# Kernel tuning notes

Measured on AMD Instinct MI355X. Metric: run time of the kernel, lower is better.

## Reference

```python
import jax, jax.numpy as jnp
import numpy as np

B = 32        # num graphs
N = 512       # nodes per graph (equal-sized blocks)
HID = 512     # hidden_dim
H = 8         # num_heads
E = 262144    # num edges
ED = 16       # edge feature dim


def setup_inputs() -> dict:
    key = jax.random.key(0)
    ks = jax.random.split(key, 12)
    x = jax.random.normal(ks[0], (B * N, HID), jnp.float32)
    # contiguous, sorted graph assignment (equal-sized graphs)
    batch = jnp.repeat(jnp.arange(B, dtype=jnp.int64), N)
    # within-graph random edges
    g = jax.random.randint(ks[1], (E,), 0, B)
    src = g * N + jax.random.randint(ks[2], (E,), 0, N)
    dst = g * N + jax.random.randint(ks[3], (E,), 0, N)
    edge_index = jnp.stack([src, dst]).astype(jnp.int64)
    edge_attr = jax.random.normal(ks[4], (E, ED), jnp.float32)
    s = 1.0 / np.sqrt(HID).astype(np.float32)
    Wq = jax.random.normal(ks[5], (HID, HID), jnp.float32) * s
    Wk = jax.random.normal(ks[6], (HID, HID), jnp.float32) * s
    Wv = jax.random.normal(ks[7], (HID, HID), jnp.float32) * s
    Wo = jax.random.normal(ks[8], (HID, HID), jnp.float32) * s
    We = jax.random.normal(ks[9], (ED, H), jnp.float32) * (1.0 / np.sqrt(ED).astype(np.float32))
    bq = jnp.zeros((HID,), jnp.float32)
    bk = jnp.zeros((HID,), jnp.float32)
    bv = jnp.zeros((HID,), jnp.float32)
    bo = jnp.zeros((HID,), jnp.float32)
    be = jnp.zeros((H,), jnp.float32)
    return dict(x=x, batch=batch, edge_index=edge_index, edge_attr=edge_attr,
                Wq=Wq, bq=bq, Wk=Wk, bk=bk, Wv=Wv, bv=bv, Wo=Wo, bo=bo,
                We=We, be=be, num_graphs=B)


def reference(x, batch, edge_index, edge_attr, Wq, bq, Wk, bk, Wv, bv, Wo, bo, We, be, num_graphs):
    n_total, hid = x.shape
    n = n_total // num_graphs           # nodes per graph (equal blocks)
    hd = hid // H                       # head_dim
    scale = 1.0 / jnp.sqrt(jnp.asarray(hd, x.dtype))
    q = (x @ Wq + bq).reshape(num_graphs, n, H, hd)
    k = (x @ Wk + bk).reshape(num_graphs, n, H, hd)
    v = (x @ Wv + bv).reshape(num_graphs, n, H, hd)
    # per-graph dense scores: [B, n(query), m(key), H]
    attn = jnp.einsum('bnhd,bmhd->bnmh', q, k) * scale
    # edge-bias scatter-add (edges are intra-graph; local coords via div/mod)
    eb = edge_attr @ We + be                      # [E, H]
    b_idx = edge_index[0] // n
    loc_src = edge_index[0] % n
    loc_dst = edge_index[1] % n
    attn = attn.at[b_idx, loc_src, loc_dst].add(eb)
    # softmax over key axis (torch dim=1 of 'nmh' == axis 2 here)
    attn = jax.nn.softmax(attn, axis=2)
    out = jnp.einsum('bnmh,bmhd->bnhd', attn, v).reshape(n_total, hid)
    return out @ Wo + bo
```

## Files before the change

### kernel.cpp

```cpp
#include <hip/hip_runtime.h>
#include <stdint.h>

typedef unsigned short u16;
typedef __bf16 bf16x8 __attribute__((ext_vector_type(8)));
typedef short  short8 __attribute__((ext_vector_type(8)));
typedef float  f32x4  __attribute__((ext_vector_type(4)));
typedef float  float4v __attribute__((ext_vector_type(4)));
typedef uint32_t u32x2 __attribute__((ext_vector_type(2)));

#define NG    32
#define NPG   512
#define HIDD  512
#define NH    8
#define HD    64
#define NE    262144
#define NNODE (NG*NPG)

__device__ __forceinline__ float fexp2(float x) { return __builtin_amdgcn_exp2f(x); }

__device__ __forceinline__ u16 f2bf(float f) {
  union { float f; uint32_t u; } x; x.f = f;
  uint32_t r = x.u + 0x7FFFu + ((x.u >> 16) & 1u);
  return (u16)(r >> 16);
}
__device__ __forceinline__ float bf2f(u16 b) {
  union { uint32_t u; float f; } x; x.u = ((uint32_t)b) << 16;
  return x.f;
}
__device__ __forceinline__ uint32_t pkbf(float a, float b) {
  __bf16 x = (__bf16)a, y = (__bf16)b;
  return (uint32_t)__builtin_bit_cast(u16, x) | ((uint32_t)__builtin_bit_cast(u16, y) << 16);
}
__device__ __forceinline__ bf16x8 ldfrag(const u16* p) {
  short8 t = *(const short8*)p;
  return __builtin_bit_cast(bf16x8, t);
}
__device__ __forceinline__ f32x4 mfma16(bf16x8 a, bf16x8 b, f32x4 c) {
  return __builtin_amdgcn_mfma_f32_16x16x32_bf16(a, b, c, 0, 0, 0);
}
__device__ __forceinline__ void gl2lds16(const void* g, void* l) {
  __builtin_amdgcn_global_load_lds((const __attribute__((address_space(1))) void*)g,
                                   (__attribute__((address_space(3))) void*)l, 16, 0, 0);
}
__device__ __forceinline__ void st(u16* p, float v)   { *p = f2bf(v); }
__device__ __forceinline__ void st(float* p, float v) { *p = v; }


__global__ void k_cast_x(const float* __restrict__ x, u16* __restrict__ xb) {
  size_t i = ((size_t)blockIdx.x * 256 + threadIdx.x) * 8;
  float4v v0 = *(const float4v*)(x + i);
  float4v v1 = *(const float4v*)(x + i + 4);
  short8 r;
  r[0]=(short)f2bf(v0[0]); r[1]=(short)f2bf(v0[1]); r[2]=(short)f2bf(v0[2]); r[3]=(short)f2bf(v0[3]);
  r[4]=(short)f2bf(v1[0]); r[5]=(short)f2bf(v1[1]); r[6]=(short)f2bf(v1[2]); r[7]=(short)f2bf(v1[3]);
  *(short8*)(xb + i) = r;
}

__global__ void k_transw(const float* __restrict__ W0, const float* __restrict__ W1,
                         const float* __restrict__ W2, const float* __restrict__ W3,
                         u16* __restrict__ wt) {
  const float* W = blockIdx.z==0 ? W0 : blockIdx.z==1 ? W1 : blockIdx.z==2 ? W2 : W3;
  u16* out = wt + (size_t)blockIdx.z * HIDD * HIDD;
  __shared__ float tl[32][33];
  int tx = threadIdx.x, ty = threadIdx.y;
  int x0 = blockIdx.x * 32, y0 = blockIdx.y * 32;
  #pragma unroll
  for (int i = 0; i < 4; ++i) tl[ty + i*8][tx] = W[(size_t)(y0 + ty + i*8) * HIDD + x0 + tx];
  __syncthreads();
  #pragma unroll
  for (int i = 0; i < 4; ++i) out[(size_t)(x0 + ty + i*8) * HIDD + (y0 + tx)] = f2bf(tl[tx][ty + i*8]);
}

__global__ void k_count2(const int* __restrict__ ei, int* __restrict__ counts) {
  int e = blockIdx.x * 256 + threadIdx.x;
  int src = ei[e];
  int dl  = ei[NE + e] & (NPG - 1);
  atomicAdd(&counts[src * 8 + (dl >> 6)], 1);
}

__global__ void k_scan_a(const int* __restrict__ counts, int* __restrict__ rowstart,
                         int* __restrict__ bsum) {
  __shared__ int arr[256];
  int t = threadIdx.x;
  int i = blockIdx.x * 256 + t;
  int c = counts[i];
  arr[t] = c;
  __syncthreads();
  for (int off = 1; off < 256; off <<= 1) {
    int v = (t >= off) ? arr[t - off] : 0;
    __syncthreads();
    arr[t] += v;
    __syncthreads();
  }
  rowstart[i] = arr[t] - c;
  if (t == 255) bsum[blockIdx.x] = arr[255];
}
__global__ void k_scan_b(int* __restrict__ bsum) {
  __shared__ int arr[512];
  int t = threadIdx.x;
  int c = bsum[t];
  arr[t] = c;
  __syncthreads();
  for (int off = 1; off < 512; off <<= 1) {
    int v = (t >= off) ? arr[t - off] : 0;
    __syncthreads();
    arr[t] += v;
    __syncthreads();
  }
  bsum[t] = arr[t] - c;
}
__global__ void k_scan_c(const int* __restrict__ bsum, int* __restrict__ rowstart) {
  int i = blockIdx.x * 256 + threadIdx.x;
  rowstart[i] += bsum[blockIdx.x];
  if (i == 0) rowstart[131072] = NE;
}

__global__ void k_fill(const int* __restrict__ ei, const float* __restrict__ ea,
                       const float* __restrict__ We, const float* __restrict__ be,
                       const int* __restrict__ rowstart, int* __restrict__ cursor,
                       uint32_t* __restrict__ packed) {
  __shared__ float w[128];
  __shared__ float bb[8];
  int t = threadIdx.x;
  if (t < 128) w[t] = We[t];
  if (t < 8)   bb[t] = be[t];
  __syncthreads();
  int e = blockIdx.x * 256 + t;
  int src = ei[e];
  int dl  = ei[NE + e] & (NPG - 1);
  const float* ap = ea + (size_t)e * 16;
  float a[16];
  #pragma unroll
  for (int i = 0; i < 16; i += 4) {
    float4v v = *(const float4v*)(ap + i);
    a[i]=v[0]; a[i+1]=v[1]; a[i+2]=v[2]; a[i+3]=v[3];
  }
  float acc[8];
  #pragma unroll
  for (int hh = 0; hh < 8; ++hh) acc[hh] = bb[hh];
  #pragma unroll
  for (int d = 0; d < 16; ++d)
    #pragma unroll
    for (int hh = 0; hh < 8; ++hh) acc[hh] += a[d] * w[d*8 + hh];
  int bin = src * 8 + (dl >> 6);
  int pos = atomicAdd(&cursor[bin], 1);
  size_t base = ((size_t)(rowstart[bin] + pos)) * 8;
  #pragma unroll
  for (int hh = 0; hh < 8; ++hh) {
    float m = fexp2(acc[hh] * 1.44269504089f);
    union { _Float16 hf; u16 us; } cv; cv.hf = (_Float16)m;
    packed[base + hh] = (uint32_t)(dl & 63) | ((uint32_t)cv.us << 16);
  }
}


template <typename OT, bool VOUT>
__device__ void gemm_body(u16* smem, const u16* __restrict__ A, const u16* __restrict__ Bt,
                          const float* __restrict__ bias, OT* __restrict__ C,
                          u16* __restrict__ vtg) {
  const int tid = threadIdx.x;
  const int w = tid >> 6, l = tid & 63, lr = l & 15, lg = l >> 4;
  const int bm0 = blockIdx.y * 128, bn0 = blockIdx.x * 128;
  const int wr = w >> 1, wc = w & 1;
  f32x4 acc[4][4];
  #pragma unroll
  for (int i = 0; i < 4; ++i)
    #pragma unroll
    for (int j = 0; j < 4; ++j) acc[i][j] = (f32x4){0.f, 0.f, 0.f, 0.f};

  const int o1 = w * 1024 + l * 16;
  auto stageAB = [&](int kt, int buf) {
    #pragma unroll
    for (int rnd = 0; rnd < 2; ++rnd) {
      const int o = rnd * 4096 + o1;
      const int row = o >> 6, colb = o & 63;
      gl2lds16((const char*)A  + ((size_t)(bm0 + row) * HIDD + kt * 32) * 2 + colb,
               (char*)smem + buf * 8192 + o);
      gl2lds16((const char*)Bt + ((size_t)(bn0 + row) * HIDD + kt * 32) * 2 + colb,
               (char*)smem + 16384 + buf * 8192 + o);
    }
  };

  stageAB(0, 0);
  for (int kt = 0; kt < 16; ++kt) {
    if (kt < 15) {
      stageAB(kt + 1, (kt + 1) & 1);
      asm volatile("s_waitcnt vmcnt(4)" ::: "memory");
    } else {
      asm volatile("s_waitcnt vmcnt(0)" ::: "memory");
    }
    __syncthreads();
    const u16* Ab = smem + (kt & 1) * 4096;
    const u16* Bb = smem + 8192 + (kt & 1) * 4096;
    bf16x8 af[4], bfr[4];
    #pragma unroll
    for (int i = 0; i < 4; ++i) af[i]  = ldfrag(&Ab[(wr*64 + i*16 + lr) * 32 + lg*8]);
    #pragma unroll
    for (int j = 0; j < 4; ++j) bfr[j] = ldfrag(&Bb[(wc*64 + j*16 + lr) * 32 + lg*8]);
    #pragma unroll
    for (int i = 0; i < 4; ++i)
      #pragma unroll
      for (int j = 0; j < 4; ++j)
        acc[i][j] = mfma16(af[i], bfr[j], acc[i][j]);
    __syncthreads();
  }

  if constexpr (VOUT) {
    #pragma unroll
    for (int j = 0; j < 4; ++j) {
      const int d = j * 16 + lr;
      const float bv = bias[bn0 + wc*64 + j*16 + lr];
      #pragma unroll
      for (int i = 0; i < 4; ++i) {
        const int t4 = wc * 2 + wr;
        const int byteo = t4 * 8192 + d * 128 + ((i*32 + lg*8) ^ ((d & 7) << 4));
        uint32_t lo = pkbf(acc[i][j][0] + bv, acc[i][j][1] + bv);
        uint32_t hi = pkbf(acc[i][j][2] + bv, acc[i][j][3] + bv);
        *(u32x2*)((char*)smem + byteo) = (u32x2){lo, hi};
      }
    }
    __syncthreads();
    const int b = bm0 >> 9, kt0 = (bm0 & 511) >> 6, h0 = bn0 >> 6;
    #pragma unroll
    for (int t4 = 0; t4 < 4; ++t4) {
      size_t base = ((size_t)(b * 8 + h0 + (t4 >> 1)) * 8 + kt0 + (t4 & 1)) * 4096;
      #pragma unroll
      for (int rnd = 0; rnd < 2; ++rnd) {
        int idx = rnd * 256 + tid;
        *(short8*)(vtg + base + idx * 8) = *(const short8*)&smem[t4 * 4096 + idx * 8];
      }
    }
  } else {
    #pragma unroll
    for (int j = 0; j < 4; ++j) {
      const int col = bn0 + wc*64 + j*16 + lr;
      const float bv = bias[col];
      #pragma unroll
      for (int i = 0; i < 4; ++i) {
        const int row0 = bm0 + wr*64 + i*16 + lg*4;
        #pragma unroll
        for (int q = 0; q < 4; ++q)
          st(&C[(size_t)(row0 + q) * HIDD + col], acc[i][j][q] + bv);
      }
    }
  }
}

__global__ __launch_bounds__(256, 3) void k_gemm_qkv(
    const u16* __restrict__ A, const u16* __restrict__ Wt,
    const float* __restrict__ b0, const float* __restrict__ b1, const float* __restrict__ b2,
    u16* __restrict__ O0, u16* __restrict__ O1, u16* __restrict__ vtg) {
  __shared__ u16 smem[16384];
  int z = blockIdx.z;
  const u16* Bt = Wt + (size_t)z * HIDD * HIDD;
  if (z == 0)      gemm_body<u16, false>(smem, A, Bt, b0, O0, nullptr);
  else if (z == 1) gemm_body<u16, false>(smem, A, Bt, b1, O1, nullptr);
  else             gemm_body<u16, true >(smem, A, Bt, b2, nullptr, vtg);
}

__global__ __launch_bounds__(256, 3) void k_gemm_out(
    const u16* __restrict__ A, const u16* __restrict__ Bt,
    const float* __restrict__ bias, float* __restrict__ C) {
  __shared__ u16 smem[16384];
  gemm_body<float, false>(smem, A, Bt, bias, C, nullptr);
}


__global__ __launch_bounds__(256, 6) void k_attn(
    const u16* __restrict__ qb, const u16* __restrict__ kb, const u16* __restrict__ vtg,
    const uint32_t* __restrict__ packed, const int* __restrict__ rowstart2,
    u16* __restrict__ ab) {
  __shared__ u16 kl[4096];
  __shared__ u16 vl[4096];
  __shared__ u16 pl[4][1024];
  const int tid = threadIdx.x, w = tid >> 6, l = tid & 63, lr = l & 15, lg = l >> 4;

  const int id = blockIdx.x;
  const int nid = (id & 7) * 256 + (id >> 3);
  const int q0 = (nid & 7) * 64;
  const int h  = (nid >> 3) & 7;
  const int b  = nid >> 6;
  const int bh = b * 8 + h;
  const int row = w * 16 + lr;
  const int grow = b * NPG + q0 + row;
  u16* plw = &pl[w][0];
  const int pswz = (lr & 7) << 4;

  bf16x8 qf[2];
  {
    const u16* qp = qb + (size_t)grow * HIDD + h * HD + lg * 8;
    qf[0] = ldfrag(qp);
    qf[1] = ldfrag(qp + 32);
  }

  auto stageK = [&](int kt) {
    #pragma unroll
    for (int rnd = 0; rnd < 2; ++rnd) {
      int o = rnd * 4096 + w * 1024 + l * 16;
      int key = o >> 7, db = o & 127;
      int col = db ^ ((key & 7) << 4);
      gl2lds16((const char*)kb + ((size_t)(b * NPG + kt * 64 + key) * HIDD + h * HD) * 2 + col,
               (char*)kl + o);
    }
  };
  auto stageV = [&](int kt) {
    #pragma unroll
    for (int rnd = 0; rnd < 2; ++rnd) {
      int o = rnd * 4096 + w * 1024 + l * 16;
      gl2lds16((const char*)vtg + ((size_t)(bh * 8 + kt)) * 8192 + o,
               (char*)vl + o);
    }
  };

  const float c1 = 0.125f * 1.44269504089f;
  float m2 = -1e30f;
  float rowsum = 0.f;
  f32x4 oacc[4];
  #pragma unroll
  for (int dt = 0; dt < 4; ++dt) oacc[dt] = (f32x4){0.f, 0.f, 0.f, 0.f};

  stageK(0); stageV(0);

  int eA = rowstart2[grow * 8];
  int eB = rowstart2[grow * 8 + 1];

  for (int kt = 0; kt < 8; ++kt) {
    asm volatile("s_waitcnt vmcnt(0)" ::: "memory");
    __syncthreads();

    int eC = (kt < 7) ? rowstart2[grow * 8 + kt + 2] : 0;
    int s0c = (eA < eB) ? eA : 0;
    uint32_t u0 = packed[(size_t)s0c * 8 + h];

    f32x4 s4[4];
    __builtin_amdgcn_s_setprio(1);
    #pragma unroll
    for (int sub = 0; sub < 4; ++sub) {
      s4[sub] = (f32x4){0.f, 0.f, 0.f, 0.f};
      int key = sub * 16 + lr;
      #pragma unroll
      for (int ks = 0; ks < 2; ++ks) {
        int db = ((ks * 32 + lg * 8) * 2) ^ ((key & 7) << 4);
        bf16x8 kf = ldfrag(&kl[(key * 128 + db) >> 1]);
        s4[sub] = mfma16(kf, qf[ks], s4[sub]);
      }
    }
    __builtin_amdgcn_s_setprio(0);

    float tm = s4[0][0];
    #pragma unroll
    for (int sub = 0; sub < 4; ++sub)
      #pragma unroll
      for (int e = 0; e < 4; ++e) tm = fmaxf(tm, s4[sub][e]);
    tm = fmaxf(tm, __shfl_xor(tm, 16, 64));
    tm = fmaxf(tm, __shfl_xor(tm, 32, 64));
    float tmc = tm * c1;
    if (__any(tmc > m2 + 8.0f)) {
      float m2n = fmaxf(m2, tmc);
      float rsc = fexp2(m2 - m2n);
      m2 = m2n;
      rowsum *= rsc;
      #pragma unroll
      for (int dt = 0; dt < 4; ++dt) oacc[dt] *= rsc;
    }

    #pragma unroll
    for (int sub = 0; sub < 4; ++sub) {
      float p0 = fexp2(__builtin_fmaf(s4[sub][0], c1, -m2));
      float p1 = fexp2(__builtin_fmaf(s4[sub][1], c1, -m2));
      float p2 = fexp2(__builtin_fmaf(s4[sub][2], c1, -m2));
      float p3 = fexp2(__builtin_fmaf(s4[sub][3], c1, -m2));
      rowsum += (p0 + p1) + (p2 + p3);
      uint32_t lo = pkbf(p0, p1);
      uint32_t hi = pkbf(p2, p3);
      *(u32x2*)((char*)plw + lr * 128 + ((sub * 32 + lg * 8) ^ pswz)) = (u32x2){lo, hi};
    }
    asm volatile("s_waitcnt lgkmcnt(0)" ::: "memory");
    __builtin_amdgcn_sched_barrier(0);

    {
      float delta = 0.f;
      uint32_t u = u0;
      for (int s = eA; s < eB; ++s) {
        uint32_t ucur = u;
        if (s + 1 < eB) u = packed[(size_t)(s + 1) * 8 + h];
        int dl = (int)(ucur & 63u);
        if ((dl & 3) == lg) {
          union { u16 us; _Float16 hf; } cv; cv.us = (u16)(ucur >> 16);
          float mult = (float)cv.hf;
          int idx = (lr * 128 + ((dl * 2) ^ pswz)) >> 1;
          float old = bf2f(plw[idx]);
          u16 nb = f2bf(old * mult);
          plw[idx] = nb;
          delta += bf2f(nb) - old;
        }
      }
      rowsum += delta;
    }
    asm volatile("s_waitcnt lgkmcnt(0)" ::: "memory");
    __builtin_amdgcn_sched_barrier(0);

    __builtin_amdgcn_s_setprio(1);
    #pragma unroll
    for (int ks = 0; ks < 2; ++ks) {
      bf16x8 pa = ldfrag(&plw[(lr * 128 + ((ks * 64 + lg * 16) ^ pswz)) >> 1]);
      #pragma unroll
      for (int dt = 0; dt < 4; ++dt) {
        int d = dt * 16 + lr;
        bf16x8 vf = ldfrag(&vl[(d * 128 + ((ks * 64 + lg * 16) ^ ((d & 7) << 4))) >> 1]);
        oacc[dt] = mfma16(vf, pa, oacc[dt]);
      }
    }
    __builtin_amdgcn_s_setprio(0);

    __syncthreads();
    if (kt < 7) { stageK(kt + 1); stageV(kt + 1); }
    eA = eB; eB = eC;
  }

  float tot = rowsum + __shfl_xor(rowsum, 16, 64);
  tot += __shfl_xor(tot, 32, 64);
  float inv = 1.0f / tot;
  #pragma unroll
  for (int dt = 0; dt < 4; ++dt) {
    uint32_t lo = pkbf(oacc[dt][0] * inv, oacc[dt][1] * inv);
    uint32_t hi = pkbf(oacc[dt][2] * inv, oacc[dt][3] * inv);
    *(u32x2*)(ab + (size_t)grow * HIDD + h * HD + dt * 16 + lg * 4) = (u32x2){lo, hi};
  }
}


extern "C" void kernel_launch(void* const* d_in, const int* in_sizes, int n_in,
                              void* d_out, int out_size, void* d_ws, size_t ws_size,
                              hipStream_t stream) {
  const float* x  = (const float*)d_in[0];
  const int*   ei = (const int*)d_in[2];
  const float* ea = (const float*)d_in[3];
  const float* Wq = (const float*)d_in[4];  const float* bq = (const float*)d_in[5];
  const float* Wk = (const float*)d_in[6];  const float* bk = (const float*)d_in[7];
  const float* Wv = (const float*)d_in[8];  const float* bv = (const float*)d_in[9];
  const float* Wo = (const float*)d_in[10]; const float* bo = (const float*)d_in[11];
  const float* We = (const float*)d_in[12]; const float* be = (const float*)d_in[13];

  char* ws = (char*)d_ws;
  const size_t MB = 1 << 20;
  u16*  xb  = (u16*)(ws);
  u16*  wt  = (u16*)(ws + 16*MB);
  u16*  qbp = (u16*)(ws + 18*MB);
  u16*  kbp = (u16*)(ws + 34*MB);
  u16*  vtg = (u16*)(ws + 50*MB);
  uint32_t* packed = (uint32_t*)(ws + 66*MB);
  int*  rowstart2 = (int*)(ws + 74*MB);
  int*  bsum      = (int*)(ws + 74*MB + 640*1024);
  int*  counts2  = (int*)(ws + 50*MB);
  int*  cursor2  = (int*)(ws + 50*MB + 512*1024);
  u16*  ab = xb;

  (void)hipMemsetAsync(counts2, 0, 2 * 512 * 1024, stream);

  k_cast_x<<<dim3(NNODE * HIDD / (256 * 8)), 256, 0, stream>>>(x, xb);
  k_transw<<<dim3(16, 16, 4), dim3(32, 8, 1), 0, stream>>>(Wq, Wk, Wv, Wo, wt);
  k_count2<<<dim3(NE / 256), 256, 0, stream>>>(ei, counts2);
  k_scan_a<<<dim3(512), 256, 0, stream>>>(counts2, rowstart2, bsum);
  k_scan_b<<<dim3(1), 512, 0, stream>>>(bsum);
  k_scan_c<<<dim3(512), 256, 0, stream>>>(bsum, rowstart2);
  k_fill<<<dim3(NE / 256), 256, 0, stream>>>(ei, ea, We, be, rowstart2, cursor2, packed);

  k_gemm_qkv<<<dim3(HIDD / 128, NNODE / 128, 3), 256, 0, stream>>>(
      xb, wt, bq, bk, bv, qbp, kbp, vtg);

  k_attn<<<dim3(2048), 256, 0, stream>>>(qbp, kbp, vtg, packed, rowstart2, ab);

  k_gemm_out<<<dim3(HIDD / 128, NNODE / 128, 1), 256, 0, stream>>>(
      ab, wt + (size_t)3 * HIDD * HIDD, bo, (float*)d_out);
}
```

Baseline: 179.7 us.

## Process 32 query rows per wave in attention to reuse K/V tiles

Each attention wave now handles two 16-row query groups instead of one, so a block covers 128 query rows and the grid halves to 1024 blocks. K and V fragments loaded from LDS are reused across both groups, and K/V global staging per query row is halved. The edge-bias loop is re-split so lane groups cover both row groups with a parity-based column class. In exchange, register pressure rises (occupancy hint drops from 6 to 4 blocks), LDS for P doubles, and fewer blocks are available to fill the GPU.

```diff
diff --git a/kernel.cpp b/kernel.cpp
--- a/kernel.cpp
+++ b/kernel.cpp
@@ -266,31 +266,31 @@
 }
 
 
-__global__ __launch_bounds__(256, 6) void k_attn(
+__global__ __launch_bounds__(256, 4) void k_attn(
     const u16* __restrict__ qb, const u16* __restrict__ kb, const u16* __restrict__ vtg,
     const uint32_t* __restrict__ packed, const int* __restrict__ rowstart2,
     u16* __restrict__ ab) {
   __shared__ u16 kl[4096];
   __shared__ u16 vl[4096];
-  __shared__ u16 pl[4][1024];
+  __shared__ u16 pl[4][2048];
   const int tid = threadIdx.x, w = tid >> 6, l = tid & 63, lr = l & 15, lg = l >> 4;
 
   const int id = blockIdx.x;
-  const int nid = (id & 7) * 256 + (id >> 3);
-  const int q0 = (nid & 7) * 64;
-  const int h  = (nid >> 3) & 7;
-  const int b  = nid >> 6;
+  const int nid = (id & 7) * 128 + (id >> 3);
+  const int q0 = (nid & 3) * 128;
+  const int h  = (nid >> 2) & 7;
+  const int b  = nid >> 5;
   const int bh = b * 8 + h;
-  const int row = w * 16 + lr;
-  const int grow = b * NPG + q0 + row;
+  const int rbase = q0 + w * 32;
   u16* plw = &pl[w][0];
   const int pswz = (lr & 7) << 4;
 
-  bf16x8 qf[2];
-  {
-    const u16* qp = qb + (size_t)grow * HIDD + h * HD + lg * 8;
-    qf[0] = ldfrag(qp);
-    qf[1] = ldfrag(qp + 32);
+  bf16x8 qf[2][2];
+  #pragma unroll
+  for (int g = 0; g < 2; ++g) {
+    const u16* qp = qb + (size_t)(b * NPG + rbase + g * 16 + lr) * HIDD + h * HD + lg * 8;
+    qf[g][0] = ldfrag(qp);
+    qf[g][1] = ldfrag(qp + 32);
   }
 
   auto stageK = [&](int kt) {
@@ -313,89 +313,111 @@
   };
 
   const float c1 = 0.125f * 1.44269504089f;
-  float m2 = -1e30f;
-  float rowsum = 0.f;
-  f32x4 oacc[4];
-  #pragma unroll
-  for (int dt = 0; dt < 4; ++dt) oacc[dt] = (f32x4){0.f, 0.f, 0.f, 0.f};
+  float m2[2] = {-1e30f, -1e30f};
+  float rs[2] = {0.f, 0.f};
+  f32x4 oacc[2][4];
+  #pragma unroll
+  for (int g = 0; g < 2; ++g)
+    #pragma unroll
+    for (int dt = 0; dt < 4; ++dt) oacc[g][dt] = (f32x4){0.f, 0.f, 0.f, 0.f};
 
   stageK(0); stageV(0);
 
-  int eA = rowstart2[grow * 8];
-  int eB = rowstart2[grow * 8 + 1];
+  const int ge = lg & 1, ecls = lg >> 1;
+  const int egrow = b * NPG + rbase + ge * 16 + lr;
+  int eA = rowstart2[egrow * 8];
+  int eB = rowstart2[egrow * 8 + 1];
 
   for (int kt = 0; kt < 8; ++kt) {
     asm volatile("s_waitcnt vmcnt(0)" ::: "memory");
     __syncthreads();
 
-    int eC = (kt < 7) ? rowstart2[grow * 8 + kt + 2] : 0;
+    int eC = (kt < 7) ? rowstart2[egrow * 8 + kt + 2] : 0;
     int s0c = (eA < eB) ? eA : 0;
     uint32_t u0 = packed[(size_t)s0c * 8 + h];
 
-    f32x4 s4[4];
+    f32x4 s4[2][4];
     __builtin_amdgcn_s_setprio(1);
     #pragma unroll
     for (int sub = 0; sub < 4; ++sub) {
-      s4[sub] = (f32x4){0.f, 0.f, 0.f, 0.f};
       int key = sub * 16 + lr;
-      #pragma unroll
-      for (int ks = 0; ks < 2; ++ks) {
-        int db = ((ks * 32 + lg * 8) * 2) ^ ((key & 7) << 4);
-        bf16x8 kf = ldfrag(&kl[(key * 128 + db) >> 1]);
-        s4[sub] = mfma16(kf, qf[ks], s4[sub]);
+      bf16x8 kf0, kf1;
+      {
+        int db0 = ((lg * 8) * 2) ^ ((key & 7) << 4);
+        int db1 = ((32 + lg * 8) * 2) ^ ((key & 7) << 4);
+        kf0 = ldfrag(&kl[(key * 128 + db0) >> 1]);
+        kf1 = ldfrag(&kl[(key * 128 + db1) >> 1]);
+      }
+      #pragma unroll
+      for (int g = 0; g < 2; ++g) {
+        s4[g][sub] = mfma16(kf0, qf[g][0], (f32x4){0.f, 0.f, 0.f, 0.f});
+        s4[g][sub] = mfma16(kf1, qf[g][1], s4[g][sub]);
       }
     }
     __builtin_amdgcn_s_setprio(0);
 
-    float tm = s4[0][0];
-    #pragma unroll
-    for (int sub = 0; sub < 4; ++sub)
-      #pragma unroll
-      for (int e = 0; e < 4; ++e) tm = fmaxf(tm, s4[sub][e]);
-    tm = fmaxf(tm, __shfl_xor(tm, 16, 64));
-    tm = fmaxf(tm, __shfl_xor(tm, 32, 64));
-    float tmc = tm * c1;
-    if (__any(tmc > m2 + 8.0f)) {
-      float m2n = fmaxf(m2, tmc);
-      float rsc = fexp2(m2 - m2n);
-      m2 = m2n;
-      rowsum *= rsc;
-      #pragma unroll
-      for (int dt = 0; dt < 4; ++dt) oacc[dt] *= rsc;
-    }
-
-    #pragma unroll
-    for (int sub = 0; sub < 4; ++sub) {
-      float p0 = fexp2(__builtin_fmaf(s4[sub][0], c1, -m2));
-      float p1 = fexp2(__builtin_fmaf(s4[sub][1], c1, -m2));
-      float p2 = fexp2(__builtin_fmaf(s4[sub][2], c1, -m2));
-      float p3 = fexp2(__builtin_fmaf(s4[sub][3], c1, -m2));
-      rowsum += (p0 + p1) + (p2 + p3);
-      uint32_t lo = pkbf(p0, p1);
-      uint32_t hi = pkbf(p2, p3);
-      *(u32x2*)((char*)plw + lr * 128 + ((sub * 32 + lg * 8) ^ pswz)) = (u32x2){lo, hi};
+    float tmc[2];
+    #pragma unroll
+    for (int g = 0; g < 2; ++g) {
+      float tm = s4[g][0][0];
+      #pragma unroll
+      for (int sub = 0; sub < 4; ++sub)
+        #pragma unroll
+        for (int e = 0; e < 4; ++e) tm = fmaxf(tm, s4[g][sub][e]);
+      tm = fmaxf(tm, __shfl_xor(tm, 16, 64));
+      tm = fmaxf(tm, __shfl_xor(tm, 32, 64));
+      tmc[g] = tm * c1;
+    }
+    if (__any(fmaxf(tmc[0] - m2[0], tmc[1] - m2[1]) > 8.0f)) {
+      #pragma unroll
+      for (int g = 0; g < 2; ++g) {
+        float m2n = fmaxf(m2[g], tmc[g]);
+        float rsc = fexp2(m2[g] - m2n);
+        m2[g] = m2n;
+        rs[g] *= rsc;
+        #pragma unroll
+        for (int dt = 0; dt < 4; ++dt) oacc[g][dt] *= rsc;
+      }
+    }
+
+    #pragma unroll
+    for (int g = 0; g < 2; ++g) {
+      const int prow = g * 16 + lr;
+      #pragma unroll
+      for (int sub = 0; sub < 4; ++sub) {
+        float p0 = fexp2(__builtin_fmaf(s4[g][sub][0], c1, -m2[g]));
+        float p1 = fexp2(__builtin_fmaf(s4[g][sub][1], c1, -m2[g]));
+        float p2 = fexp2(__builtin_fmaf(s4[g][sub][2], c1, -m2[g]));
+        float p3 = fexp2(__builtin_fmaf(s4[g][sub][3], c1, -m2[g]));
+        rs[g] += (p0 + p1) + (p2 + p3);
+        uint32_t lo = pkbf(p0, p1);
+        uint32_t hi = pkbf(p2, p3);
+        *(u32x2*)((char*)plw + prow * 128 + ((sub * 32 + lg * 8) ^ pswz)) = (u32x2){lo, hi};
+      }
     }
     asm volatile("s_waitcnt lgkmcnt(0)" ::: "memory");
     __builtin_amdgcn_sched_barrier(0);
 
     {
       float delta = 0.f;
+      const int re = ge * 16 + lr;
       uint32_t u = u0;
       for (int s = eA; s < eB; ++s) {
         uint32_t ucur = u;
         if (s + 1 < eB) u = packed[(size_t)(s + 1) * 8 + h];
         int dl = (int)(ucur & 63u);
-        if ((dl & 3) == lg) {
+        if ((dl & 1) == ecls) {
           union { u16 us; _Float16 hf; } cv; cv.us = (u16)(ucur >> 16);
           float mult = (float)cv.hf;
-          int idx = (lr * 128 + ((dl * 2) ^ pswz)) >> 1;
+          int idx = (re * 128 + ((dl * 2) ^ pswz)) >> 1;
           float old = bf2f(plw[idx]);
           u16 nb = f2bf(old * mult);
           plw[idx] = nb;
           delta += bf2f(nb) - old;
         }
       }
-      rowsum += delta;
+      rs[0] += (ge == 0) ? delta : 0.f;
+      rs[1] += (ge == 1) ? delta : 0.f;
     }
     asm volatile("s_waitcnt lgkmcnt(0)" ::: "memory");
     __builtin_amdgcn_sched_barrier(0);
@@ -403,12 +425,14 @@
     __builtin_amdgcn_s_setprio(1);
     #pragma unroll
     for (int ks = 0; ks < 2; ++ks) {
-      bf16x8 pa = ldfrag(&plw[(lr * 128 + ((ks * 64 + lg * 16) ^ pswz)) >> 1]);
+      bf16x8 pa0 = ldfrag(&plw[(lr * 128 + ((ks * 64 + lg * 16) ^ pswz)) >> 1]);
+      bf16x8 pa1 = ldfrag(&plw[((16 + lr) * 128 + ((ks * 64 + lg * 16) ^ pswz)) >> 1]);
       #pragma unroll
       for (int dt = 0; dt < 4; ++dt) {
         int d = dt * 16 + lr;
         bf16x8 vf = ldfrag(&vl[(d * 128 + ((ks * 64 + lg * 16) ^ ((d & 7) << 4))) >> 1]);
-        oacc[dt] = mfma16(vf, pa, oacc[dt]);
+        oacc[0][dt] = mfma16(vf, pa0, oacc[0][dt]);
+        oacc[1][dt] = mfma16(vf, pa1, oacc[1][dt]);
       }
     }
     __builtin_amdgcn_s_setprio(0);
@@ -418,14 +442,18 @@
     eA = eB; eB = eC;
   }
 
-  float tot = rowsum + __shfl_xor(rowsum, 16, 64);
-  tot += __shfl_xor(tot, 32, 64);
-  float inv = 1.0f / tot;
-  #pragma unroll
-  for (int dt = 0; dt < 4; ++dt) {
-    uint32_t lo = pkbf(oacc[dt][0] * inv, oacc[dt][1] * inv);
-    uint32_t hi = pkbf(oacc[dt][2] * inv, oacc[dt][3] * inv);
-    *(u32x2*)(ab + (size_t)grow * HIDD + h * HD + dt * 16 + lg * 4) = (u32x2){lo, hi};
+  #pragma unroll
+  for (int g = 0; g < 2; ++g) {
+    float tot = rs[g] + __shfl_xor(rs[g], 16, 64);
+    tot += __shfl_xor(tot, 32, 64);
+    float inv = 1.0f / tot;
+    const size_t grow = (size_t)(b * NPG + rbase + g * 16 + lr);
+    #pragma unroll
+    for (int dt = 0; dt < 4; ++dt) {
+      uint32_t lo = pkbf(oacc[g][dt][0] * inv, oacc[g][dt][1] * inv);
+      uint32_t hi = pkbf(oacc[g][dt][2] * inv, oacc[g][dt][3] * inv);
+      *(u32x2*)(ab + grow * HIDD + h * HD + dt * 16 + lg * 4) = (u32x2){lo, hi};
+    }
   }
 }
 
@@ -469,7 +497,7 @@
   k_gemm_qkv<<<dim3(HIDD / 128, NNODE / 128, 3), 256, 0, stream>>>(
       xb, wt, bq, bk, bv, qbp, kbp, vtg);
 
-  k_attn<<<dim3(2048), 256, 0, stream>>>(qbp, kbp, vtg, packed, rowstart2, ab);
+  k_attn<<<dim3(1024), 256, 0, stream>>>(qbp, kbp, vtg, packed, rowstart2, ab);
 
   k_gemm_out<<<dim3(HIDD / 128, NNODE / 128, 1), 256, 0, stream>>>(
       ab, wt + (size_t)3 * HIDD * HIDD, bo, (float*)d_out);
```

New measurement: 165.9 us. 7.7% less time.
